# Optimization experiments

Measured on AMD Instinct MI355X. Metric: run time of the kernel, lower is better.

Reference implementation:

```python
import jax, jax.numpy as jnp
import numpy as np

B, C, H, W = 8, 768, 64, 64
BOT = 64   # bottleneck_dim
PD = 96    # prompt_dim
KP = 32    # number of prompt tokens
KK = 9     # 3x3 kernel points


def gelu(x):
    return jax.nn.gelu(x, approximate=False)  # torch nn.GELU default (erf)


def layernorm(x, g, b, eps=1e-5):
    m = jnp.mean(x, axis=-1, keepdims=True)
    v = jnp.var(x, axis=-1, keepdims=True)
    return (x - m) * jax.lax.rsqrt(v + eps) * g + b


def conv3x3(x, w, b):
    # x [B,Ci,H,W], w [Co,Ci,3,3] (torch layout), stride 1, pad 1
    y = jax.lax.conv_general_dilated(x, w, (1, 1), ((1, 1), (1, 1)))
    return y + b[None, :, None, None]


def deform_conv3x3(x, offset, w, pad=1):
    # mmcv DeformConv2d (v1, no mask, bias=False), deform_groups=1.
    # x [B,Ci,H,W]; offset [B,2*KK,H,W] in (dy,dx) pairs per kernel point.
    Bn, Ci, Hn, Wn = x.shape
    Co = w.shape[0]
    off = offset.reshape(Bn, KK, 2, Hn, Wn)
    dy, dx = off[:, :, 0], off[:, :, 1]                      # [B,KK,H,W]
    ky, kx = jnp.meshgrid(jnp.arange(3), jnp.arange(3), indexing='ij')
    py = (jnp.arange(Hn, dtype=x.dtype)[None, None, :, None] - pad
          + ky.reshape(1, KK, 1, 1).astype(x.dtype) + dy)    # sample rows
    px = (jnp.arange(Wn, dtype=x.dtype)[None, None, None, :] - pad
          + kx.reshape(1, KK, 1, 1).astype(x.dtype) + dx)    # sample cols
    y0 = jnp.floor(py)
    x0 = jnp.floor(px)
    wy = (py - y0)[:, None]                                   # [B,1,KK,H,W]
    wx = (px - x0)[:, None]
    xf = x.reshape(Bn, Ci, Hn * Wn)
    y0i = y0.astype(jnp.int32)
    x0i = x0.astype(jnp.int32)

    def samp(yi, xi):
        valid = ((yi >= 0) & (yi < Hn) & (xi >= 0) & (xi < Wn))
        yc = jnp.clip(yi, 0, Hn - 1)
        xc = jnp.clip(xi, 0, Wn - 1)
        idx = (yc * Wn + xc).reshape(Bn, -1)                  # [B,KK*H*W]
        g = jax.vmap(lambda f, i: f[:, i])(xf, idx)           # [B,Ci,KK*H*W]
        g = g.reshape(Bn, Ci, KK, Hn, Wn)
        return g * valid[:, None].astype(x.dtype)

    g00 = samp(y0i, x0i)
    g01 = samp(y0i, x0i + 1)
    g10 = samp(y0i + 1, x0i)
    g11 = samp(y0i + 1, x0i + 1)
    val = (g00 * (1 - wy) * (1 - wx) + g01 * (1 - wy) * wx
           + g10 * wy * (1 - wx) + g11 * wy * wx)             # [B,Ci,KK,H,W]
    return jnp.einsum('bckhw,ock->bohw', val, w.reshape(Co, Ci, KK))


def setup_inputs() -> dict:
    key = jax.random.key(0)
    ks = jax.random.split(key, 16)
    s = 0.02
    inp = {
        'x': jax.random.normal(ks[0], (B, C, H, W), jnp.float32),
        'irf': jax.random.normal(ks[1], (B, BOT, H, W), jnp.float32),
        'tf': jax.random.normal(ks[2], (KP, PD), jnp.float32),
        'ln_g': jnp.ones((C,), jnp.float32),
        'ln_b': jnp.zeros((C,), jnp.float32),
        'Wd': jax.random.normal(ks[3], (C, BOT), jnp.float32) * s,
        'bd': jnp.zeros((BOT,), jnp.float32),
        'Wu': jax.random.normal(ks[4], (BOT, C), jnp.float32) * s,
        'bu': jnp.zeros((C,), jnp.float32),
        'off_w': jax.random.normal(ks[5], (2 * KK, 2 * BOT, 3, 3), jnp.float32) * s,
        'off_b': jnp.zeros((2 * KK,), jnp.float32),
        'mod_w1': jax.random.normal(ks[6], (BOT // 4, BOT), jnp.float32) * s,
        'mod_b1': jnp.zeros((BOT // 4,), jnp.float32),
        'mod_w2': jax.random.normal(ks[7], (BOT, BOT // 4), jnp.float32) * s,
        'mod_b2': jnp.zeros((BOT,), jnp.float32),
        'dc_w': jax.random.normal(ks[8], (BOT, BOT, 3, 3), jnp.float32) * s,
        'alpha': jnp.full((1,), 0.1, jnp.float32),
        'Wk': jax.random.normal(ks[9], (PD, C), jnp.float32) * s,
        'bk': jnp.zeros((C,), jnp.float32),
        'Wv': jax.random.normal(ks[10], (PD, C), jnp.float32) * s,
        'bv': jnp.zeros((C,), jnp.float32),
        'temperature': jnp.full((1,), 0.07, jnp.float32),
        'Wg1': jax.random.normal(ks[11], (C, C // 4), jnp.float32) * s,
        'bg1': jnp.zeros((C // 4,), jnp.float32),
        'Wg2': jax.random.normal(ks[12], (C // 4, 1), jnp.float32) * s,
        'bg2': jnp.zeros((1,), jnp.float32),
        'scale': jnp.full((1,), 0.1, jnp.float32),
    }
    return inp


def reference(x, irf, tf, ln_g, ln_b, Wd, bd, Wu, bu, off_w, off_b,
              mod_w1, mod_b1, mod_w2, mod_b2, dc_w, alpha,
              Wk, bk, Wv, bv, temperature, Wg1, bg1, Wg2, bg2, scale):
    identity = x
    xp = jnp.transpose(x, (0, 2, 3, 1))                       # [B,H,W,C]
    x_down = gelu(layernorm(xp, ln_g, ln_b) @ Wd + bd)        # [B,H,W,BOT]
    # --- IRRGBFuse ---
    xc = jnp.transpose(x_down, (0, 3, 1, 2))                  # [B,BOT,H,W]
    offset = conv3x3(jnp.concatenate([xc, irf], axis=1), off_w, off_b)
    x_def = deform_conv3x3(xc, offset, dc_w)                  # [B,BOT,H,W]
    m = jnp.einsum('bchw,oc->bohw', irf, mod_w1) + mod_b1[None, :, None, None]
    m = jnp.einsum('bchw,oc->bohw', gelu(m), mod_w2) + mod_b2[None, :, None, None]
    m = jax.nn.sigmoid(m)
    x_fused = x_def + alpha * (x_def * m)
    x_fused = jnp.transpose(x_fused, (0, 2, 3, 1))            # [B,H,W,BOT]
    # --- up-projection + residual (dropout inactive in eval) ---
    x_up = x_fused @ Wu + bu
    x_res1 = xp + scale * x_up                                # [B,H,W,C]
    x_flat = x_res1.reshape(B, H * W, C)
    # --- cosine cross-attention over prompts ---
    pk = tf @ Wk + bk                                          # [K,C]
    pv = tf @ Wv + bv
    xn = x_flat / jnp.maximum(jnp.linalg.norm(x_flat, axis=-1, keepdims=True), 1e-12)
    pkn = pk / jnp.maximum(jnp.linalg.norm(pk, axis=-1, keepdims=True), 1e-12)
    cos = jnp.einsum('bnc,kc->bnk', xn, pkn)
    attn = jax.nn.softmax(cos / temperature, axis=-1)
    x_prompted = jnp.einsum('bnk,kc->bnc', attn, pv).reshape(B, H, W, C)
    # --- gate + residuals ---
    g = jax.nn.sigmoid(gelu(x_res1 @ Wg1 + bg1) @ Wg2 + bg2)   # [B,H,W,1]
    x_gated = x_res1 + g * x_prompted
    return identity + scale * jnp.transpose(x_gated, (0, 3, 1, 2))
```

## Files before the change

### kernel.cpp

```cpp
#include <hip/hip_runtime.h>
#include <hip/hip_bf16.h>
#include <math.h>

#define BN 8
#define C 768
#define H 64
#define W 64
#define HW 4096
#define BOT 64
#define PD 96
#define KP 32
#define KKN 9
#define NPX (BN*HW)

typedef __hip_bfloat16 bf16;
typedef __attribute__((ext_vector_type(8))) short bf16x8;
typedef __attribute__((ext_vector_type(4))) float f32x4;
#define MFMA16(a,b,c) __builtin_amdgcn_mfma_f32_16x16x32_bf16(a,b,c,0,0,0)

__device__ __forceinline__ float gelu_f(float x) {
    return 0.5f * x * (1.0f + erff(x * 0.70710678118654752440f));
}
__device__ __forceinline__ float sigmoid_f(float x) {
    return 1.0f / (1.0f + __expf(-x));
}
__device__ __forceinline__ float bf2f(short s) {
    return __uint_as_float(((unsigned)(unsigned short)s) << 16);
}

__global__ void k_prep(const float* __restrict__ Wd, const float* __restrict__ ln_g,
                       const float* __restrict__ ln_b, const float* __restrict__ bd,
                       const float* __restrict__ off_w, const float* __restrict__ dc_w,
                       const float* __restrict__ Wg1, const float* __restrict__ Wu,
                       const float* __restrict__ tf, const float* __restrict__ Wk,
                       const float* __restrict__ bk, const float* __restrict__ Wv,
                       const float* __restrict__ bv,
                       bf16* __restrict__ wdt, float* __restrict__ s12,
                       bf16* __restrict__ off_wt, bf16* __restrict__ dcb2,
                       bf16* __restrict__ wg1bt, bf16* __restrict__ wut,
                       float* __restrict__ pk, float* __restrict__ pvout) {
    int bx = blockIdx.x;
    int tid = threadIdx.x;
    if (bx < 192) {
        int i = bx*256 + tid;
        if (i < C*BOT) {
            int c = i >> 6, o = i & 63;
            wdt[(size_t)o*C + c] = __float2bfloat16(ln_g[c] * Wd[(size_t)c*BOT + o]);
        }
    } else if (bx == 192) {
        __shared__ float p1[4][64], p2[4][64];
        int o = tid & 63, part = tid >> 6;
        float a1 = 0.f, a2 = 0.f;
        for (int c = part; c < C; c += 4) {
            float wv = Wd[(size_t)c*BOT + o];
            a1 += ln_g[c] * wv;
            a2 += ln_b[c] * wv;
        }
        p1[part][o] = a1; p2[part][o] = a2;
        __syncthreads();
        if (tid < 64) {
            s12[o]      = p1[0][o]+p1[1][o]+p1[2][o]+p1[3][o];
            s12[64 + o] = p2[0][o]+p2[1][o]+p2[2][o]+p2[3][o] + bd[o];
        }
    } else if (bx < 337) {
        int i = (bx-193)*256 + tid;
        if (i < 32*1152) {
            int o = i / 1152, kk = i % 1152;
            int k = kk >> 7, ci = kk & 127;
            float v = (o < 18) ? off_w[(size_t)(o*128 + ci)*9 + k] : 0.0f;
            off_wt[i] = __float2bfloat16(v);
        }
    } else if (bx < 481) {
        int i = (bx-337)*256 + tid;
        if (i < 36864) {
            int e = i & 7;
            int lane = (i >> 3) & 63;
            int s = (i >> 9) & 1;
            int f = (i >> 10) & 3;
            int k = i >> 12;
            int lg = lane >> 4, lm = lane & 15;
            int o = f*16 + lm;
            int ci = s*32 + lg*8 + e;
            dcb2[i] = __float2bfloat16(dc_w[((size_t)o*64 + ci)*9 + k]);
        }
    } else if (bx < 1057) {
        int i = (bx-481)*256 + tid;
        if (i < 192*C) {
            int h = i / C, c = i % C;
            wg1bt[i] = __float2bfloat16(Wg1[(size_t)c*192 + h]);
        }
    } else if (bx < 1249) {
        int i = (bx-1057)*256 + tid;
        if (i < C*BOT) {
            int c = i >> 6, k = i & 63;
            wut[i] = __float2bfloat16(Wu[(size_t)k*C + c]);
        }
    } else {
        int i = (bx-1249)*256 + tid;
        if (i < KP*C) {
            int k = i / C, c = i % C;
            float aK = bk[c], aV = bv[c];
            for (int p = 0; p < PD; p++) {
                float tv = tf[k*PD+p];
                aK += tv * Wk[(size_t)p*C + c];
                aV += tv * Wv[(size_t)p*C + c];
            }
            pk[i] = aK; pvout[i] = aV;
        }
    }
}

__global__ void k_down_fused(const float* __restrict__ x, const bf16* __restrict__ wdt,
                             const float* __restrict__ s12, bf16* __restrict__ catb) {
    int blk = blockIdx.x;
    int b = blk >> 6; int hw0 = (blk & 63) * 64;
    int w = threadIdx.x >> 6, lane = threadIdx.x & 63;
    int lg = lane >> 4, lm = lane & 15;
    int pix = hw0 + w*16 + lm;
    const float* xb = x + (size_t)b*C*HW + pix;
    f32x4 acc[4];
#pragma unroll
    for (int f = 0; f < 4; f++) acc[f] = (f32x4){0.f,0.f,0.f,0.f};
    float ssum = 0.f, sqsum = 0.f;
#pragma unroll 2
    for (int kk = 0; kk < 24; kk++) {
        int cbase = kk*32 + lg*8;
        float xv[8];
#pragma unroll
        for (int e = 0; e < 8; e++) {
            xv[e] = xb[(size_t)(cbase + e)*HW];
            ssum += xv[e];
            sqsum += xv[e]*xv[e];
        }
        union { bf16 h[8]; bf16x8 v; } ub;
#pragma unroll
        for (int e = 0; e < 8; e++) ub.h[e] = __float2bfloat16(xv[e]);
#pragma unroll
        for (int f = 0; f < 4; f++) {
            bf16x8 a = *(const bf16x8*)(wdt + (size_t)(f*16 + lm)*C + cbase);
            acc[f] = MFMA16(a, ub.v, acc[f]);
        }
    }
    ssum  += __shfl_xor(ssum, 16);  ssum  += __shfl_xor(ssum, 32);
    sqsum += __shfl_xor(sqsum, 16); sqsum += __shfl_xor(sqsum, 32);
    float mean = ssum * (1.0f/C);
    float var  = sqsum * (1.0f/C) - mean*mean;
    float rstd = rsqrtf(var + 1e-5f);
    bf16* dst = catb + (size_t)(b*HW + pix)*128;
#pragma unroll
    for (int f = 0; f < 4; f++) {
        union { bf16 h[4]; uint2 q; } u;
#pragma unroll
        for (int r = 0; r < 4; r++) {
            int o = f*16 + lg*4 + r;
            float y = rstd*(acc[f][r] - mean*s12[o]) + s12[64 + o];
            u.h[r] = __float2bfloat16(gelu_f(y));
        }
        *(uint2*)(dst + f*16 + lg*4) = u.q;
    }
}

__global__ void k_mod(const float* __restrict__ irf, const float* __restrict__ w1, const float* __restrict__ b1,
                      const float* __restrict__ w2, const float* __restrict__ b2,
                      bf16* __restrict__ mbf, bf16* __restrict__ catb) {
    int blk = blockIdx.x;
    int b = blk >> 6; int hw0 = (blk & 63)*64;
    int px = threadIdx.x & 63;
    int g = threadIdx.x >> 6;
    __shared__ float tile[64][64];
    __shared__ float hid[16][64];
    const float* ib = irf + (size_t)b*BOT*HW + hw0;
#pragma unroll
    for (int i = 0; i < 16; i++) {
        int ci = g + 4*i;
        tile[ci][px] = ib[(size_t)ci*HW + px];
    }
    __syncthreads();
    {
        int xp = threadIdx.x >> 2, q = threadIdx.x & 3;
        union { bf16 h[16]; uint4 v[2]; } u2;
#pragma unroll
        for (int i = 0; i < 16; i++) u2.h[i] = __float2bfloat16(tile[q*16 + i][xp]);
        uint4* d2 = (uint4*)(catb + (size_t)(b*HW + hw0 + xp)*128 + 64 + q*16);
        d2[0] = u2.v[0]; d2[1] = u2.v[1];
    }
#pragma unroll
    for (int jj = 0; jj < 4; jj++) {
        int j = g*4 + jj;
        float a = b1[j];
        for (int ci = 0; ci < 64; ci++) a += tile[ci][px] * w1[j*64+ci];
        hid[j][px] = gelu_f(a);
    }
    __syncthreads();
    union { bf16 h[16]; uint4 q[2]; } u;
#pragma unroll
    for (int s = 0; s < 16; s++) {
        int o = g*16 + s;
        float a = b2[o];
#pragma unroll
        for (int j = 0; j < 16; j++) a += hid[j][px] * w2[o*16+j];
        u.h[s] = __float2bfloat16(sigmoid_f(a));
    }
    uint4* dst = (uint4*)(mbf + (size_t)(b*HW + hw0 + px)*64 + g*16);
    dst[0] = u.q[0]; dst[1] = u.q[1];
}

__global__ void k_offconv_mfma(const bf16* __restrict__ catb, const bf16* __restrict__ off_wt,
                               const float* __restrict__ off_b, float* __restrict__ offs) {
    int blk = blockIdx.x;
    int b = blk >> 6, y = blk & 63;
    int tid = threadIdx.x;
    __shared__ uint4 lds4[3072];
    char* lds = (char*)lds4;
#pragma unroll
    for (int it = 0; it < 12; it++) {
        int idx = it*256 + tid;
        int ci8 = idx & 15, xx = (idx >> 4) & 63, lr = idx >> 10;
        int yy = y - 1 + lr;
        uint4 v = {0u,0u,0u,0u};
        if (yy >= 0 && yy < H)
            v = *(const uint4*)(catb + (size_t)(b*HW + yy*64 + xx)*128 + ci8*8);
        int lofs = (lr*16384 + xx*256) | ((ci8*16) ^ ((xx & 15) << 4));
        *(uint4*)(lds + lofs) = v;
    }
    __syncthreads();
    int w = tid >> 6, lane = tid & 63;
    int lg = lane >> 4, lm = lane & 15;
    f32x4 acc0 = {0.f,0.f,0.f,0.f}, acc1 = {0.f,0.f,0.f,0.f};
    const bf16* brow0 = off_wt + (size_t)lm*1152;
    const bf16* brow1 = off_wt + (size_t)(16+lm)*1152;
#pragma unroll
    for (int k = 0; k < 9; k++) {
        int ky = k/3, kx = k%3;
        int xs = w*16 + lm + kx - 1;
        bool valid = (xs >= 0 && xs < 64);
        int rowbase = ky*16384 + xs*256;
        int sw = (xs & 15) << 4;
#pragma unroll
        for (int ci0 = 0; ci0 < 128; ci0 += 32) {
            bf16x8 a = {0,0,0,0,0,0,0,0};
            if (valid) a = *(const bf16x8*)(lds + (rowbase | ((ci0*2 + lg*16) ^ sw)));
            bf16x8 bb0 = *(const bf16x8*)(brow0 + k*128 + ci0 + lg*8);
            bf16x8 bb1 = *(const bf16x8*)(brow1 + k*128 + ci0 + lg*8);
            acc0 = MFMA16(a, bb0, acc0);
            acc1 = MFMA16(a, bb1, acc1);
        }
    }
    float bi0 = off_b[lm];
    float bi1 = (lm < 2) ? off_b[16+lm] : 0.f;
#pragma unroll
    for (int r = 0; r < 4; r++) {
        int pr = w*16 + lg*4 + r;
        offs[(size_t)(b*18 + lm)*HW + y*64 + pr] = acc0[r] + bi0;
        if (lm < 2)
            offs[(size_t)(b*18 + 16 + lm)*HW + y*64 + pr] = acc1[r] + bi1;
    }
}

__global__ void k_deform_mfma(const bf16* __restrict__ catb, const float* __restrict__ offs,
                              const bf16* __restrict__ dcb2, const bf16* __restrict__ mbf,
                              const float* __restrict__ alpha, bf16* __restrict__ xfb) {
    int blk = blockIdx.x;
    int b = blk >> 6, y = blk & 63;
    int tid = threadIdx.x;
    __shared__ int   sy0[9][64];
    __shared__ int   sx0[9][64];
    __shared__ float swy[9][64];
    __shared__ float swx[9][64];
    for (int item = tid; item < 576; item += 256) {
        int k = item >> 6, xx = item & 63;
        float dy = offs[(size_t)(b*18 + 2*k  )*HW + y*W + xx];
        float dx = offs[(size_t)(b*18 + 2*k+1)*HW + y*W + xx];
        float py  = (float)(y  - 1 + k/3) + dy;
        float pxf = (float)(xx - 1 + k%3) + dx;
        float fy = floorf(py), fx = floorf(pxf);
        sy0[k][xx] = (int)fy;
        sx0[k][xx] = (int)fx;
        swy[k][xx] = py - fy;
        swx[k][xx] = pxf - fx;
    }
    __syncthreads();
    int w = tid >> 6, lane = tid & 63;
    int lg = lane >> 4, lm = lane & 15;
    int pix = w*16 + lm;
    const bf16* cb = catb + (size_t)b*HW*128;
    f32x4 acc[4];
#pragma unroll
    for (int f = 0; f < 4; f++) acc[f] = (f32x4){0.f,0.f,0.f,0.f};
#pragma unroll
    for (int k = 0; k < 9; k++) {
        int y0 = sy0[k][pix], x0 = sx0[k][pix];
        float wy = swy[k][pix], wx = swx[k][pix];
        bool vy0 = (y0 >= 0 && y0 < H), vy1 = (y0+1 >= 0 && y0+1 < H);
        bool vx0 = (x0 >= 0 && x0 < W), vx1 = (x0+1 >= 0 && x0+1 < W);
        float va[16];
#pragma unroll
        for (int i = 0; i < 16; i++) va[i] = 0.f;
#pragma unroll
        for (int cy = 0; cy < 2; cy++) {
#pragma unroll
            for (int cx = 0; cx < 2; cx++) {
                bool v = (cy ? vy1 : vy0) && (cx ? vx1 : vx0);
                if (v) {
                    float wc = (cy ? wy : (1.f-wy)) * (cx ? wx : (1.f-wx));
                    const bf16* base = cb + (size_t)((y0+cy)*64 + (x0+cx))*128;
                    bf16x8 v0 = *(const bf16x8*)(base + lg*8);
                    bf16x8 v1 = *(const bf16x8*)(base + 32 + lg*8);
#pragma unroll
                    for (int e = 0; e < 8; e++) {
                        va[e]   += wc * bf2f(v0[e]);
                        va[8+e] += wc * bf2f(v1[e]);
                    }
                }
            }
        }
        union { bf16 h[8]; bf16x8 v; } ua0, ua1;
#pragma unroll
        for (int e = 0; e < 8; e++) {
            ua0.h[e] = __float2bfloat16(va[e]);
            ua1.h[e] = __float2bfloat16(va[8+e]);
        }
        const bf16* dk = dcb2 + ((size_t)k*8*64 + lane)*8;
#pragma unroll
        for (int f = 0; f < 4; f++) {
            bf16x8 b0 = *(const bf16x8*)(dk + (size_t)(f*2+0)*64*8);
            bf16x8 b1 = *(const bf16x8*)(dk + (size_t)(f*2+1)*64*8);
            acc[f] = MFMA16(ua0.v, b0, acc[f]);
            acc[f] = MFMA16(ua1.v, b1, acc[f]);
        }
    }
    float al = alpha[0];
    const bf16* mrow = mbf + (size_t)(b*HW + y*64)*64;
    bf16* xrow = xfb + (size_t)(b*HW + y*64)*64;
    int prow = w*16 + lg*4;
#pragma unroll
    for (int f = 0; f < 4; f++) {
        int o = f*16 + lm;
#pragma unroll
        for (int r = 0; r < 4; r++) {
            int p = prow + r;
            float mm = __bfloat162float(mrow[(size_t)p*64 + o]);
            xrow[(size_t)p*64 + o] = __float2bfloat16(acc[f][r] * (1.f + al*mm));
        }
    }
}

__global__ void k_up_mfma(const float* __restrict__ x, const bf16* __restrict__ xfb,
                          const bf16* __restrict__ wut, const float* __restrict__ bu,
                          const float* __restrict__ scale, bf16* __restrict__ xres1) {
    int blk = blockIdx.x;
    int b = blk >> 6; int hw0 = (blk & 63)*64;
    int c00 = blockIdx.y * 192;
    int w = threadIdx.x >> 6, lane = threadIdx.x & 63;
    int lg = lane >> 4, lm = lane & 15;
    int prow = hw0 + w*16;
    const bf16* arow = xfb + (size_t)(b*HW + prow + lm)*BOT;
    bf16x8 a0 = *(const bf16x8*)(arow + lg*8);
    bf16x8 a1 = *(const bf16x8*)(arow + 32 + lg*8);
    float sc = scale[0];
    const float* xb = x + (size_t)b*C*HW;
    bf16* xrb = xres1 + (size_t)(b*HW)*C;
#pragma unroll 3
    for (int n0 = c00; n0 < c00 + 192; n0 += 64) {
        f32x4 acc[4];
#pragma unroll
        for (int f = 0; f < 4; f++) {
            int ncol = n0 + f*16 + lm;
            bf16x8 b0 = *(const bf16x8*)(wut + (size_t)ncol*BOT + lg*8);
            bf16x8 b1 = *(const bf16x8*)(wut + (size_t)ncol*BOT + 32 + lg*8);
            f32x4 t = {0.f,0.f,0.f,0.f};
            t = MFMA16(a0, b0, t);
            t = MFMA16(a1, b1, t);
            acc[f] = t;
        }
#pragma unroll
        for (int f = 0; f < 4; f++) {
            int c = n0 + f*16 + lm;
            float bias = bu[c];
#pragma unroll
            for (int r = 0; r < 4; r++) {
                int pix = prow + lg*4 + r;
                float xv = xb[(size_t)c*HW + pix];
                float rv = xv + sc*(acc[f][r] + bias);
                xrb[(size_t)pix*C + c] = __float2bfloat16(rv);
            }
        }
    }
}

__global__ void k_promptfin(const float* __restrict__ pk, const float* __restrict__ pv,
                            bf16* __restrict__ pkn, bf16* __restrict__ pvt) {
    if (blockIdx.x == 96) {
        __shared__ float part[32][9];
        __shared__ float rn[32];
        int t = threadIdx.x;
        int k = t >> 3, sl = t & 7;
        float s = 0.f;
        for (int c = sl; c < C; c += 8) { float v = pk[(size_t)k*C+c]; s += v*v; }
        part[k][sl] = s;
        __syncthreads();
        if (t < 32) {
            float tot = 0.f;
            for (int j = 0; j < 8; j++) tot += part[t][j];
            rn[t] = 1.0f / fmaxf(sqrtf(tot), 1e-12f);
        }
        __syncthreads();
        for (int i = t; i < KP*C; i += 256) pkn[i] = __float2bfloat16(pk[i] * rn[i/C]);
    } else {
        int i = blockIdx.x*256 + threadIdx.x;
        int c = i >> 5, k = i & 31;
        pvt[i] = __float2bfloat16(pv[(size_t)k*C + c]);
    }
}

__global__ void k_attn_gate(const bf16* __restrict__ xres1, const bf16* __restrict__ pkn,
                            const float* __restrict__ temp,
                            const bf16* __restrict__ wg1bt, const float* __restrict__ bg1,
                            const float* __restrict__ Wg2, const float* __restrict__ bg2,
                            bf16* __restrict__ atb, float* __restrict__ gbuf) {
    int pix0 = blockIdx.x * 32;
    int tid = threadIdx.x;
    int w = tid >> 6, lane = tid & 63;
    int lg = lane >> 4, lm = lane & 15;
    __shared__ char xt[32*1536];
    __shared__ float gl_part[2][32];

    {
        uint4 tmp[12];
#pragma unroll
        for (int it = 0; it < 12; it++) {
            int idx = it*256 + tid;
            int row = idx / 96, c16 = idx % 96;
            tmp[it] = *(const uint4*)(xres1 + (size_t)(pix0 + row)*C + c16*8);
        }
#pragma unroll
        for (int it = 0; it < 12; it++) {
            int idx = it*256 + tid;
            int row = idx / 96, c16 = idx % 96;
            int ofs = row*1536 + ((c16*16) ^ ((row & 7) << 4));
            *(uint4*)(xt + ofs) = tmp[it];
        }
    }
    __syncthreads();

    if (w < 2) {
        int prow = pix0 + w*16;
        int lrow = w*16 + lm;
        const char* arow = xt + lrow*1536;
        int sw = (lrow & 7) << 4;
        f32x4 acc0 = {0.f,0.f,0.f,0.f}, acc1 = {0.f,0.f,0.f,0.f};
        float ssq = 0.f;
        const bf16* b0row = pkn + (size_t)lm*C;
        const bf16* b1row = pkn + (size_t)(16 + lm)*C;
#pragma unroll 4
        for (int c0 = 0; c0 < C; c0 += 32) {
            bf16x8 a  = *(const bf16x8*)(arow + ((c0*2 + lg*16) ^ sw));
            bf16x8 b0 = *(const bf16x8*)(b0row + c0 + lg*8);
            bf16x8 b1 = *(const bf16x8*)(b1row + c0 + lg*8);
#pragma unroll
            for (int e = 0; e < 8; e++) {
                float av = bf2f(a[e]);
                ssq += av*av;
            }
            acc0 = MFMA16(a, b0, acc0);
            acc1 = MFMA16(a, b1, acc1);
        }
        ssq += __shfl_xor(ssq, 16);
        ssq += __shfl_xor(ssq, 32);
        float invnv = 1.0f / fmaxf(sqrtf(ssq), 1e-12f);
        float it = 1.0f / temp[0];
#pragma unroll
        for (int r = 0; r < 4; r++) {
            int pr = lg*4 + r;
            float iv = __shfl(invnv, pr);
            float s = iv * it;
            float v0 = acc0[r]*s, v1 = acc1[r]*s;
            float m = fmaxf(v0, v1);
            m = fmaxf(m, __shfl_xor(m, 1));
            m = fmaxf(m, __shfl_xor(m, 2));
            m = fmaxf(m, __shfl_xor(m, 4));
            m = fmaxf(m, __shfl_xor(m, 8));
            float e0 = __expf(v0-m), e1 = __expf(v1-m);
            float ss = e0 + e1;
            ss += __shfl_xor(ss, 1);
            ss += __shfl_xor(ss, 2);
            ss += __shfl_xor(ss, 4);
            ss += __shfl_xor(ss, 8);
            float inv = 1.0f / ss;
            bf16* ao = atb + (size_t)(prow + pr)*KP;
            ao[lm]      = __float2bfloat16(e0*inv);
            ao[16 + lm] = __float2bfloat16(e1*inv);
        }
    } else {
        int gw = w - 2;
        f32x4 acc[2][6];
#pragma unroll
        for (int pg = 0; pg < 2; pg++)
#pragma unroll
            for (int f = 0; f < 6; f++)
                acc[pg][f] = (f32x4){0.f,0.f,0.f,0.f};
        int lrow0 = lm, lrow1 = 16 + lm;
        const char* ar0 = xt + lrow0*1536;
        const char* ar1 = xt + lrow1*1536;
        int sw0 = (lrow0 & 7) << 4;
        int sw1 = (lrow1 & 7) << 4;
        const bf16* b0 = wg1bt + (size_t)(gw*96 + lm)*C;
        for (int c0 = 0; c0 < C; c0 += 32) {
            bf16x8 a[2], bb[6];
            a[0] = *(const bf16x8*)(ar0 + ((c0*2 + lg*16) ^ sw0));
            a[1] = *(const bf16x8*)(ar1 + ((c0*2 + lg*16) ^ sw1));
#pragma unroll
            for (int f = 0; f < 6; f++)
                bb[f] = *(const bf16x8*)(b0 + (size_t)f*16*C + c0 + lg*8);
#pragma unroll
            for (int pg = 0; pg < 2; pg++)
#pragma unroll
                for (int f = 0; f < 6; f++)
                    acc[pg][f] = MFMA16(a[pg], bb[f], acc[pg][f]);
        }
        float wg2v[6], bg1v[6];
#pragma unroll
        for (int f = 0; f < 6; f++) {
            int h = gw*96 + f*16 + lm;
            wg2v[f] = Wg2[h];
            bg1v[f] = bg1[h];
        }
#pragma unroll
        for (int pg = 0; pg < 2; pg++) {
#pragma unroll
            for (int r = 0; r < 4; r++) {
                float s = 0.f;
#pragma unroll
                for (int f = 0; f < 6; f++)
                    s += gelu_f(acc[pg][f][r] + bg1v[f]) * wg2v[f];
                s += __shfl_xor(s, 1);
                s += __shfl_xor(s, 2);
                s += __shfl_xor(s, 4);
                s += __shfl_xor(s, 8);
                if (lm == 0) gl_part[gw][pg*16 + lg*4 + r] = s;
            }
        }
    }
    __syncthreads();
    if (threadIdx.x < 32) {
        float t = gl_part[0][threadIdx.x] + gl_part[1][threadIdx.x];
        gbuf[pix0 + threadIdx.x] = sigmoid_f(t + bg2[0]);
    }
}

__global__ void k_out(const float* __restrict__ x, const bf16* __restrict__ xres1,
                      const bf16* __restrict__ atb, const float* __restrict__ gbuf,
                      const bf16* __restrict__ pvt, const float* __restrict__ scale,
                      float* __restrict__ out) {
    int blk = blockIdx.x;
    int pix0 = blk * 64;
    int b = blk >> 6; int hw0 = (blk & 63) * 64;
    int c0 = blockIdx.y * 192;
    int w = threadIdx.x >> 6, lane = threadIdx.x & 63;
    int lg = lane >> 4, lm = lane & 15;
    union { bf16 h[8]; bf16x8 v; } ua;
    ua.v = *(const bf16x8*)(atb + (size_t)(pix0 + w*16 + lm)*KP + lg*8);
    float sc = scale[0];
    float gv[4];
#pragma unroll
    for (int r = 0; r < 4; r++) gv[r] = gbuf[pix0 + w*16 + lg*4 + r];
    const float* xb = x + (size_t)b*C*HW;
    float* ob = out + (size_t)b*C*HW;
    int pbase = hw0 + w*16 + lg*4;
    const bf16* xr0 = xres1 + (size_t)(pix0 + w*16 + lg*4)*C;
#pragma unroll 3
    for (int n0 = c0; n0 < c0 + 192; n0 += 64) {
#pragma unroll
        for (int f = 0; f < 4; f++) {
            int c = n0 + f*16 + lm;
            bf16x8 bfrag = *(const bf16x8*)(pvt + (size_t)c*KP + lg*8);
            f32x4 z = {0.f,0.f,0.f,0.f};
            f32x4 acc = MFMA16(ua.v, bfrag, z);
            float4 x4 = *(const float4*)(xb + (size_t)c*HW + pbase);
            float4 o4;
            float xr;
            xr = __bfloat162float(xr0[c]);
            o4.x = x4.x + sc*(xr + gv[0]*acc[0]);
            xr = __bfloat162float(xr0[C + c]);
            o4.y = x4.y + sc*(xr + gv[1]*acc[1]);
            xr = __bfloat162float(xr0[2*C + c]);
            o4.z = x4.z + sc*(xr + gv[2]*acc[2]);
            xr = __bfloat162float(xr0[3*C + c]);
            o4.w = x4.w + sc*(xr + gv[3]*acc[3]);
            *(float4*)(ob + (size_t)c*HW + pbase) = o4;
        }
    }
}

extern "C" void kernel_launch(void* const* d_in, const int* in_sizes, int n_in,
                              void* d_out, int out_size, void* d_ws, size_t ws_size,
                              hipStream_t stream) {
    const float* x      = (const float*)d_in[0];
    const float* irf    = (const float*)d_in[1];
    const float* tf     = (const float*)d_in[2];
    const float* ln_g   = (const float*)d_in[3];
    const float* ln_b   = (const float*)d_in[4];
    const float* Wd     = (const float*)d_in[5];
    const float* bd     = (const float*)d_in[6];
    const float* Wu     = (const float*)d_in[7];
    const float* bu     = (const float*)d_in[8];
    const float* off_w  = (const float*)d_in[9];
    const float* off_b  = (const float*)d_in[10];
    const float* mod_w1 = (const float*)d_in[11];
    const float* mod_b1 = (const float*)d_in[12];
    const float* mod_w2 = (const float*)d_in[13];
    const float* mod_b2 = (const float*)d_in[14];
    const float* dc_w   = (const float*)d_in[15];
    const float* alpha  = (const float*)d_in[16];
    const float* Wk     = (const float*)d_in[17];
    const float* bk     = (const float*)d_in[18];
    const float* Wv     = (const float*)d_in[19];
    const float* bv     = (const float*)d_in[20];
    const float* temp   = (const float*)d_in[21];
    const float* Wg1    = (const float*)d_in[22];
    const float* bg1    = (const float*)d_in[23];
    const float* Wg2    = (const float*)d_in[24];
    const float* bg2    = (const float*)d_in[25];
    const float* scale  = (const float*)d_in[26];
    float* out = (float*)d_out;

    char* w = (char*)d_ws;
    auto alloc = [&](size_t bytes) {
        char* p = w;
        w += (bytes + 255) & ~(size_t)255;
        return p;
    };
    float* offs  = (float*)alloc((size_t)BN*18*HW*4);
    float* pk    = (float*)alloc((size_t)KP*C*4);
    float* pv    = (float*)alloc((size_t)KP*C*4);
    float* gbuf  = (float*)alloc((size_t)NPX*4);
    float* s12   = (float*)alloc((size_t)128*4);
    bf16* xres1  = (bf16*)alloc((size_t)NPX*C*2);
    bf16* pkn    = (bf16*)alloc((size_t)KP*C*2);
    bf16* pvt    = (bf16*)alloc((size_t)C*KP*2);
    bf16* atb    = (bf16*)alloc((size_t)NPX*KP*2);
    bf16* wg1bt  = (bf16*)alloc((size_t)192*C*2);
    bf16* catb   = (bf16*)alloc((size_t)NPX*128*2);
    bf16* offwt  = (bf16*)alloc((size_t)32*1152*2);
    bf16* xfb    = (bf16*)alloc((size_t)NPX*BOT*2);
    bf16* wut    = (bf16*)alloc((size_t)C*BOT*2);
    bf16* mbf    = (bf16*)alloc((size_t)NPX*BOT*2);
    bf16* dcb2   = (bf16*)alloc((size_t)36864*2);
    bf16* wdt    = (bf16*)alloc((size_t)C*BOT*2);

    k_prep<<<1345, 256, 0, stream>>>(Wd, ln_g, ln_b, bd, off_w, dc_w, Wg1, Wu,
                                     tf, Wk, bk, Wv, bv,
                                     wdt, s12, offwt, dcb2, wg1bt, wut, pk, pv);
    k_down_fused<<<512, 256, 0, stream>>>(x, wdt, s12, catb);
    k_mod<<<512, 256, 0, stream>>>(irf, mod_w1, mod_b1, mod_w2, mod_b2, mbf, catb);
    k_offconv_mfma<<<512, 256, 0, stream>>>(catb, offwt, off_b, offs);
    k_deform_mfma<<<512, 256, 0, stream>>>(catb, offs, dcb2, mbf, alpha, xfb);
    k_up_mfma<<<dim3(512,4), 256, 0, stream>>>(x, xfb, wut, bu, scale, xres1);
    k_promptfin<<<97, 256, 0, stream>>>(pk, pv, pkn, pvt);
    k_attn_gate<<<1024, 256, 0, stream>>>(xres1, pkn, temp,
                                          wg1bt, bg1, Wg2, bg2, atb, gbuf);
    k_out<<<dim3(512,4), 256, 0, stream>>>(x, xres1, atb, gbuf, pvt, scale, out);
}
```

Measured before the change: 314.6 us.

## Split down-projection across warps by output tile with LDS double-buffered input

The down-projection kernel now gives each block 16 pixels instead of 64, and each warp computes one 16-column slice of the 64 outputs instead of all four slices. The block stages the input channels into a double-buffered shared tile using float2 loads, and all warps read the same tile. The grid grows from 512 to 2048 blocks to raise parallelism and memory-level concurrency on the 100MB input read. In exchange each pixel's input is loaded into shared memory once and reused by four warps, and a __syncthreads is added on every channel step. The LayerNorm statistics are now computed redundantly in every warp.

```diff
diff --git a/kernel.cpp b/kernel.cpp
--- a/kernel.cpp
+++ b/kernel.cpp
@@ -112,52 +112,58 @@
 
 __global__ void k_down_fused(const float* __restrict__ x, const bf16* __restrict__ wdt,
                              const float* __restrict__ s12, bf16* __restrict__ catb) {
-    int blk = blockIdx.x;
-    int b = blk >> 6; int hw0 = (blk & 63) * 64;
-    int w = threadIdx.x >> 6, lane = threadIdx.x & 63;
+    int gpix = blockIdx.x * 16;
+    int b = gpix >> 12;
+    int hw0 = gpix & 4095;
+    int tid = threadIdx.x;
+    int w = tid >> 6, lane = tid & 63;
     int lg = lane >> 4, lm = lane & 15;
-    int pix = hw0 + w*16 + lm;
-    const float* xb = x + (size_t)b*C*HW + pix;
-    f32x4 acc[4];
-#pragma unroll
-    for (int f = 0; f < 4; f++) acc[f] = (f32x4){0.f,0.f,0.f,0.f};
+    __shared__ float xt[2][32][20];
+    const float* xb = x + (size_t)b*C*HW + hw0;
+    int sc_ = tid >> 3;
+    int sp  = (tid & 7) << 1;
+    {
+        float2 v = *(const float2*)(xb + (size_t)sc_*HW + sp);
+        *(float2*)&xt[0][sc_][sp] = v;
+    }
+    __syncthreads();
+    f32x4 acc0 = {0.f,0.f,0.f,0.f};
     float ssum = 0.f, sqsum = 0.f;
-#pragma unroll 2
+    const bf16* arow = wdt + (size_t)(w*16 + lm)*C;
     for (int kk = 0; kk < 24; kk++) {
-        int cbase = kk*32 + lg*8;
+        int cur = kk & 1;
+        float2 nv;
+        if (kk < 23)
+            nv = *(const float2*)(xb + (size_t)((kk+1)*32 + sc_)*HW + sp);
         float xv[8];
 #pragma unroll
         for (int e = 0; e < 8; e++) {
-            xv[e] = xb[(size_t)(cbase + e)*HW];
-            ssum += xv[e];
-            sqsum += xv[e]*xv[e];
+            float v = xt[cur][lg*8+e][lm];
+            xv[e] = v; ssum += v; sqsum += v*v;
         }
         union { bf16 h[8]; bf16x8 v; } ub;
 #pragma unroll
         for (int e = 0; e < 8; e++) ub.h[e] = __float2bfloat16(xv[e]);
-#pragma unroll
-        for (int f = 0; f < 4; f++) {
-            bf16x8 a = *(const bf16x8*)(wdt + (size_t)(f*16 + lm)*C + cbase);
-            acc[f] = MFMA16(a, ub.v, acc[f]);
-        }
+        bf16x8 a = *(const bf16x8*)(arow + kk*32 + lg*8);
+        acc0 = MFMA16(a, ub.v, acc0);
+        if (kk < 23)
+            *(float2*)&xt[cur^1][sc_][sp] = nv;
+        __syncthreads();
     }
     ssum  += __shfl_xor(ssum, 16);  ssum  += __shfl_xor(ssum, 32);
     sqsum += __shfl_xor(sqsum, 16); sqsum += __shfl_xor(sqsum, 32);
     float mean = ssum * (1.0f/C);
     float var  = sqsum * (1.0f/C) - mean*mean;
     float rstd = rsqrtf(var + 1e-5f);
-    bf16* dst = catb + (size_t)(b*HW + pix)*128;
-#pragma unroll
-    for (int f = 0; f < 4; f++) {
-        union { bf16 h[4]; uint2 q; } u;
-#pragma unroll
-        for (int r = 0; r < 4; r++) {
-            int o = f*16 + lg*4 + r;
-            float y = rstd*(acc[f][r] - mean*s12[o]) + s12[64 + o];
-            u.h[r] = __float2bfloat16(gelu_f(y));
-        }
-        *(uint2*)(dst + f*16 + lg*4) = u.q;
-    }
+    bf16* dst = catb + (size_t)(gpix + lm)*128;
+    union { bf16 h[4]; uint2 q; } u;
+#pragma unroll
+    for (int r = 0; r < 4; r++) {
+        int o = w*16 + lg*4 + r;
+        float y = rstd*(acc0[r] - mean*s12[o]) + s12[64 + o];
+        u.h[r] = __float2bfloat16(gelu_f(y));
+    }
+    *(uint2*)(dst + w*16 + lg*4) = u.q;
 }
 
 __global__ void k_mod(const float* __restrict__ irf, const float* __restrict__ w1, const float* __restrict__ b1,
@@ -651,7 +657,7 @@
     k_prep<<<1345, 256, 0, stream>>>(Wd, ln_g, ln_b, bd, off_w, dc_w, Wg1, Wu,
                                      tf, Wk, bk, Wv, bv,
                                      wdt, s12, offwt, dcb2, wg1bt, wut, pk, pv);
-    k_down_fused<<<512, 256, 0, stream>>>(x, wdt, s12, catb);
+    k_down_fused<<<2048, 256, 0, stream>>>(x, wdt, s12, catb);
     k_mod<<<512, 256, 0, stream>>>(irf, mod_w1, mod_b1, mod_w2, mod_b2, mbf, catb);
     k_offconv_mfma<<<512, 256, 0, stream>>>(catb, offwt, off_b, offs);
     k_deform_mfma<<<512, 256, 0, stream>>>(catb, offs, dcb2, mbf, alpha, xfb);
```

After: 311.3 us. Within noise of the previous version (-1.1%).
